# Performance work log

Measured on AMD Instinct MI355X. Metric: run time of the kernel, lower is better.

## Reference

```python
import jax, jax.numpy as jnp
import numpy as np

N_NODES = 50000
N_EDGES = 1_600_000
IN_C, HID_C, OUT_C = 512, 256, 50
ALPHA = 0.1
NUM_LAYERS = 10


def setup_inputs() -> dict:
    key = jax.random.key(0)
    ks = jax.random.split(key, 8)
    x = jax.random.normal(ks[0], (N_NODES, IN_C), dtype=jnp.float32)
    edge_row = jax.random.randint(ks[1], (N_EDGES,), 0, N_NODES, dtype=jnp.int32)
    edge_col = jax.random.randint(ks[2], (N_EDGES,), 0, N_NODES, dtype=jnp.int32)
    edge_weight = jax.random.uniform(ks[3], (N_EDGES,), dtype=jnp.float32)
    s1 = 1.0 / np.sqrt(IN_C)
    s2 = 1.0 / np.sqrt(HID_C)
    W1 = jax.random.uniform(ks[4], (IN_C, HID_C), minval=-s1, maxval=s1, dtype=jnp.float32)
    b1 = jax.random.uniform(ks[5], (HID_C,), minval=-s1, maxval=s1, dtype=jnp.float32)
    W2 = jax.random.uniform(ks[6], (HID_C, OUT_C), minval=-s2, maxval=s2, dtype=jnp.float32)
    b2 = jax.random.uniform(ks[7], (OUT_C,), minval=-s2, maxval=s2, dtype=jnp.float32)
    return {"x": x, "edge_row": edge_row, "edge_col": edge_col,
            "edge_weight": edge_weight, "W1": W1, "b1": b1, "W2": W2, "b2": b2}


def reference(x, edge_row, edge_col, edge_weight, W1, b1, W2, b2):
    # MLP: Linear -> ReLU -> Linear (dropout inactive in eval, no batch norm)
    h = jax.nn.relu(x @ W1 + b1)          # [N, HID_C]
    h = h @ W2 + b2                        # [N, OUT_C]
    x0 = h

    def spmm(v):
        # out[i] = sum_{e: row[e]==i} w[e] * v[col[e]]
        msgs = v[edge_col] * edge_weight[:, None]   # [E, OUT_C]
        return jax.ops.segment_sum(msgs, edge_row, num_segments=N_NODES)

    def step(h, _):
        h = spmm(h) * (1.0 - ALPHA) + ALPHA * x0
        return h, None

    h, _ = jax.lax.scan(step, h, None, length=NUM_LAYERS)
    return jax.nn.log_softmax(h, axis=1)
```

## Files before the change

### kernel.cpp

```cpp
#include <hip/hip_runtime.h>
#include <cstddef>
#include <cstdint>
#include <math.h>

#define N_NODES 50000
#define N_EDGES 1600000
#define IN_C 512
#define HID_C 256
#define OUT_C 50
#define PAD_C 64
#define NUM_LAYERS 10
#define NBUCK 98
#define BSHIFT 9
#define BCAP 20480
#define PHB_CHUNK 8192
#define PHB_BLOCKS 196
#define TW_BLOCKS 128
#define PW_BLOCKS 64
#define GEMM_BLOCKS 782

typedef __attribute__((ext_vector_type(8))) short short8;
typedef __attribute__((ext_vector_type(4))) float floatx4;

__device__ inline unsigned short f2bf(float f) {
    unsigned int u = __float_as_uint(f);
    u += 0x7fffu + ((u >> 16) & 1u);
    return (unsigned short)(u >> 16);
}

__device__ inline unsigned cvtpk(float lo, float hi) {
    unsigned r;
    asm("v_cvt_pk_bf16_f32 %0, %1, %2" : "=v"(r) : "v"(lo), "v"(hi));
    return r;
}

__device__ inline short8 pack_bf16x8(float4 lo, float4 hi) {
    union { unsigned u[4]; short8 s; } r;
    r.u[0] = cvtpk(lo.x, lo.y);
    r.u[1] = cvtpk(lo.z, lo.w);
    r.u[2] = cvtpk(hi.x, hi.y);
    r.u[3] = cvtpk(hi.z, hi.w);
    return r.s;
}

#define ASYNC16(g, l)                                                     \
    __builtin_amdgcn_global_load_lds(                                     \
        (const __attribute__((address_space(1))) void*)(g),               \
        (__attribute__((address_space(3))) void*)(l), 16, 0, 0)

#define WAITCNT6() asm volatile("s_waitcnt vmcnt(6)" ::: "memory")
#define WAITCNT0() asm volatile("s_waitcnt vmcnt(0)" ::: "memory")
#define SBAR()     __builtin_amdgcn_s_barrier()

__global__ __launch_bounds__(256) void prep_fused(const int* __restrict__ erow,
                                                  const int* __restrict__ ecol,
                                                  const float* __restrict__ ew,
                                                  int* __restrict__ bfill,
                                                  uint2* __restrict__ buckets,
                                                  const float* __restrict__ W1,
                                                  unsigned short* __restrict__ Wt,
                                                  const float* __restrict__ W2,
                                                  const float* __restrict__ b2,
                                                  unsigned short* __restrict__ Wpt,
                                                  float* __restrict__ bp) {
    __shared__ int  lcnt[NBUCK];
    __shared__ int  lbase[NBUCK];
    __shared__ float tile[32][33];
    const int bid = blockIdx.x;
    const int t = threadIdx.x;

    if (bid < PHB_BLOCKS) {
        for (int b = t; b < NBUCK; b += 256) lcnt[b] = 0;
        __syncthreads();
        const int e0 = bid * PHB_CHUNK;
        const int e1 = min(e0 + PHB_CHUNK, N_EDGES);
        for (int e = e0 + t; e < e1; e += 256)
            atomicAdd(&lcnt[erow[e] >> BSHIFT], 1);
        __syncthreads();
        for (int b = t; b < NBUCK; b += 256) {
            lbase[b] = atomicAdd(&bfill[b], lcnt[b]);
            lcnt[b] = 0;
        }
        __syncthreads();
        for (int e = e0 + t; e < e1; e += 256) {
            int r = erow[e];
            int b = r >> BSHIFT;
            int o = atomicAdd(&lcnt[b], 1);
            int idx = lbase[b] + o;
            if (idx < BCAP) {
                unsigned packed = ((unsigned)(r - (b << BSHIFT)) << 17) | (unsigned)ecol[e];
                buckets[(size_t)b * BCAP + idx] = make_uint2(packed, __float_as_uint(ew[e]));
            }
        }
    } else if (bid < PHB_BLOCKS + TW_BLOCKS) {
        int tb = bid - PHB_BLOCKS;
        int bx = tb & 15;
        int by = tb >> 4;
        int tx = t & 31, ty = t >> 5;
#pragma unroll
        for (int i = 0; i < 32; i += 8)
            tile[ty + i][tx] = W1[(bx * 32 + ty + i) * HID_C + by * 32 + tx];
        __syncthreads();
#pragma unroll
        for (int i = 0; i < 32; i += 8)
            Wt[(size_t)(by * 32 + ty + i) * IN_C + bx * 32 + tx] = f2bf(tile[tx][ty + i]);
    } else {
        int idx = (bid - PHB_BLOCKS - TW_BLOCKS) * 256 + t;
        if (idx < PAD_C * HID_C) {
            int n = idx >> 8, k = idx & 255;
            float v = (n < OUT_C) ? W2[k * OUT_C + n] : 0.f;
            Wpt[idx] = f2bf(v);
        }
        if (idx < PAD_C) bp[idx] = (idx < OUT_C) ? b2[idx] : 0.f;
    }
}

__global__ __launch_bounds__(128) void bucket_scan(const int* __restrict__ bfill,
                                                   int* __restrict__ bbase,
                                                   int* __restrict__ rowptr) {
    __shared__ int sd[128];
    int t = threadIdx.x;
    int v = (t < NBUCK) ? min(bfill[t], BCAP) : 0;
    sd[t] = v;
    __syncthreads();
    for (int off = 1; off < 128; off <<= 1) {
        int x = (t >= off) ? sd[t - off] : 0;
        __syncthreads();
        sd[t] += x;
        __syncthreads();
    }
    if (t < NBUCK) bbase[t] = sd[t] - v;
    if (t == NBUCK - 1) {
        bbase[NBUCK] = sd[t];
        rowptr[N_NODES] = sd[t];
    }
}

__global__ __launch_bounds__(256) void csr_gemm_fused(
        const uint2* __restrict__ buckets, const int* __restrict__ bfill,
        const int* __restrict__ bbase, int* __restrict__ rowptr,
        uint2* __restrict__ edges,
        const float* __restrict__ A, const unsigned short* __restrict__ Wt,
        const float* __restrict__ b1, const unsigned short* __restrict__ Wpt,
        const float* __restrict__ bp, unsigned short* __restrict__ h0b) {
    __shared__ __align__(16) char smem[73728];
    const int bid = blockIdx.x;
    const int tid = threadIdx.x;

    if (bid < NBUCK) {
        int* hist = (int*)smem;
        int* excl = (int*)(smem + 2048);
        int* psum = (int*)(smem + 4096);
        const int b = bid;
        const int t = tid;
        const int n = min(bfill[b], BCAP);
        const uint2* bk = buckets + (size_t)b * BCAP;

        hist[t] = 0; hist[t + 256] = 0;
        __syncthreads();
        for (int i = t; i < n; i += 256)
            atomicAdd(&hist[bk[i].x >> 17], 1);
        __syncthreads();
        int a0 = hist[2 * t], a1 = hist[2 * t + 1];
        psum[t] = a0 + a1;
        __syncthreads();
        for (int off = 1; off < 256; off <<= 1) {
            int x = (t >= off) ? psum[t - off] : 0;
            __syncthreads();
            psum[t] += x;
            __syncthreads();
        }
        int pe = psum[t] - (a0 + a1);
        excl[2 * t] = pe;
        excl[2 * t + 1] = pe + a0;
        __syncthreads();
        const int base = bbase[b];
#pragma unroll
        for (int k = 0; k < 2; ++k) {
            int lr = t + k * 256;
            int r = (b << BSHIFT) + lr;
            if (r < N_NODES) rowptr[r] = base + excl[lr];
        }
        hist[t] = 0; hist[t + 256] = 0;
        __syncthreads();
        for (int i = t; i < n; i += 256) {
            uint2 ed = bk[i];
            int lr = ed.x >> 17;
            int pos = base + excl[lr] + atomicAdd(&hist[lr], 1);
            edges[pos] = make_uint2(ed.x & 0x1FFFFu, ed.y);
        }
        return;
    }

    float*          Ab[3] = {(float*)smem,
                             (float*)(smem + 24576),
                             (float*)(smem + 49152)};
    unsigned short* Bb[3] = {(unsigned short*)(smem + 8192),
                             (unsigned short*)(smem + 32768),
                             (unsigned short*)(smem + 57344)};
    unsigned short* Hs = (unsigned short*)smem;
    const int HS_LD = 264;

    const int wave = tid >> 6, lane = tid & 63;
    const int quad = lane >> 4, l16 = lane & 15;
    const int m0 = (bid - NBUCK) * 64;
    const int wm = (wave >> 1) * 32;
    const int wn = (wave & 1) * 128;

    floatx4 acc[2][8];
#pragma unroll
    for (int i = 0; i < 2; ++i)
#pragma unroll
        for (int j = 0; j < 8; ++j) acc[i][j] = (floatx4){0.f, 0.f, 0.f, 0.f};

    auto stage = [&](int bi, int ks) {
        const int k0 = ks << 5;
#pragma unroll
        for (int j = 0; j < 2; ++j) {
            int slot = tid + j * 256;
            int r = slot >> 3, c = slot & 7;
            int gr = m0 + r;
            if (gr >= N_NODES) gr = N_NODES - 1;
            const float* src = A + (size_t)gr * IN_C + k0 + ((c ^ (r & 7)) << 2);
            ASYNC16(src, Ab[bi] + (slot << 2));
        }
#pragma unroll
        for (int j = 0; j < 4; ++j) {
            int slot = tid + j * 256;
            int n = slot >> 2, c = slot & 3;
            int cs = c ^ ((n >> 1) & 3);
            const unsigned short* src = Wt + (size_t)n * IN_C + k0 + (cs << 3);
            ASYNC16(src, Bb[bi] + (slot << 3));
        }
    };

    auto compute = [&](int bi) {
        const float* As_ = Ab[bi];
        const unsigned short* Bs_ = Bb[bi];
        short8 bfr[8], afr[2];
#pragma unroll
        for (int nt = 0; nt < 8; ++nt) {
            int n  = wn + nt * 16 + l16;
            int cq = quad ^ ((n >> 1) & 3);
            bfr[nt] = *(const short8*)&Bs_[(n << 5) + (cq << 3)];
        }
#pragma unroll
        for (int mt = 0; mt < 2; ++mt) {
            int r  = wm + mt * 16 + l16;
            int rx = r & 7;
            float4 lo = *(const float4*)&As_[(r << 5) + (((2 * quad)     ^ rx) << 2)];
            float4 hi = *(const float4*)&As_[(r << 5) + (((2 * quad + 1) ^ rx) << 2)];
            afr[mt] = pack_bf16x8(lo, hi);
        }
#pragma unroll
        for (int mt = 0; mt < 2; ++mt)
#pragma unroll
            for (int nt = 0; nt < 8; ++nt)
                acc[mt][nt] = __builtin_amdgcn_mfma_f32_16x16x32_bf16(afr[mt], bfr[nt],
                                                                      acc[mt][nt], 0, 0, 0);
    };

    stage(0, 0);
    stage(1, 1);
#pragma unroll
    for (int ks = 0; ks < 14; ++ks) {
        WAITCNT6();
        SBAR();
        stage((ks + 2) % 3, ks + 2);
        compute(ks % 3);
    }
    WAITCNT6(); SBAR(); compute(2);
    WAITCNT0(); SBAR(); compute(0);
    __syncthreads();

#pragma unroll
    for (int nt = 0; nt < 8; ++nt) {
        int n = wn + nt * 16 + l16;
        float bn = b1[n];
#pragma unroll
        for (int mt = 0; mt < 2; ++mt)
#pragma unroll
            for (int r = 0; r < 4; ++r) {
                float v = acc[mt][nt][r] + bn;
                v = v > 0.f ? v : 0.f;
                Hs[(wm + mt * 16 + quad * 4 + r) * HS_LD + n] = f2bf(v);
            }
    }
    __syncthreads();

    floatx4 acc2[4];
#pragma unroll
    for (int nt = 0; nt < 4; ++nt) acc2[nt] = (floatx4){0.f, 0.f, 0.f, 0.f};
    const int hrow = (wave << 4) + l16;
#pragma unroll
    for (int k2 = 0; k2 < 8; ++k2) {
        short8 haf = *(const short8*)&Hs[hrow * HS_LD + (k2 << 5) + (quad << 3)];
#pragma unroll
        for (int nt = 0; nt < 4; ++nt) {
            short8 bf = *(const short8*)&Wpt[(size_t)((nt << 4) + l16) * HID_C + (k2 << 5) + (quad << 3)];
            acc2[nt] = __builtin_amdgcn_mfma_f32_16x16x32_bf16(haf, bf, acc2[nt], 0, 0, 0);
        }
    }
#pragma unroll
    for (int nt = 0; nt < 4; ++nt) {
        int c = (nt << 4) + l16;
        float bn = bp[c];
#pragma unroll
        for (int r = 0; r < 4; ++r) {
            int row = m0 + (wave << 4) + (quad << 2) + r;
            if (row < N_NODES)
                h0b[(size_t)row * PAD_C + c] = f2bf(acc2[nt][r] + bn);
        }
    }
}

__device__ inline void edge_fma(float* acc, float wgt, uint4 hv) {
    acc[0] = fmaf(wgt, __uint_as_float(hv.x << 16),         acc[0]);
    acc[1] = fmaf(wgt, __uint_as_float(hv.x & 0xffff0000u), acc[1]);
    acc[2] = fmaf(wgt, __uint_as_float(hv.y << 16),         acc[2]);
    acc[3] = fmaf(wgt, __uint_as_float(hv.y & 0xffff0000u), acc[3]);
    acc[4] = fmaf(wgt, __uint_as_float(hv.z << 16),         acc[4]);
    acc[5] = fmaf(wgt, __uint_as_float(hv.z & 0xffff0000u), acc[5]);
    acc[6] = fmaf(wgt, __uint_as_float(hv.w << 16),         acc[6]);
    acc[7] = fmaf(wgt, __uint_as_float(hv.w & 0xffff0000u), acc[7]);
}

template <bool LAST>
__global__ __launch_bounds__(256, 8) void prop8(const int* __restrict__ rowptr,
                                                const uint2* __restrict__ edges,
                                                const unsigned short* __restrict__ hin,
                                                const unsigned short* __restrict__ h0b,
                                                unsigned short* __restrict__ hout_b,
                                                float* __restrict__ out_f) {
    int wid = (blockIdx.x * blockDim.x + threadIdx.x) >> 6;
    if (wid >= N_NODES) return;
    int lane = threadIdx.x & 63;
    int slot = lane >> 3;
    int lc   = lane & 7;
    int s = rowptr[wid], e = rowptr[wid + 1];

    float acc0[8], acc1[8];
#pragma unroll
    for (int k = 0; k < 8; ++k) { acc0[k] = 0.f; acc1[k] = 0.f; }

    int i = s;
    for (; i + 32 <= e; i += 32) {
        uint2 cw0 = edges[i + slot];
        uint2 cw1 = edges[i + 8 + slot];
        uint2 cw2 = edges[i + 16 + slot];
        uint2 cw3 = edges[i + 24 + slot];
        uint4 hv0 = *(const uint4*)((const char*)hin + ((size_t)cw0.x << 7) + lc * 16);
        uint4 hv1 = *(const uint4*)((const char*)hin + ((size_t)cw1.x << 7) + lc * 16);
        uint4 hv2 = *(const uint4*)((const char*)hin + ((size_t)cw2.x << 7) + lc * 16);
        uint4 hv3 = *(const uint4*)((const char*)hin + ((size_t)cw3.x << 7) + lc * 16);
        edge_fma(acc0, __uint_as_float(cw0.y), hv0);
        edge_fma(acc1, __uint_as_float(cw1.y), hv1);
        edge_fma(acc0, __uint_as_float(cw2.y), hv2);
        edge_fma(acc1, __uint_as_float(cw3.y), hv3);
    }
    for (; i + 16 <= e; i += 16) {
        uint2 cw0 = edges[i + slot];
        uint2 cw1 = edges[i + 8 + slot];
        uint4 hv0 = *(const uint4*)((const char*)hin + ((size_t)cw0.x << 7) + lc * 16);
        uint4 hv1 = *(const uint4*)((const char*)hin + ((size_t)cw1.x << 7) + lc * 16);
        edge_fma(acc0, __uint_as_float(cw0.y), hv0);
        edge_fma(acc1, __uint_as_float(cw1.y), hv1);
    }
    for (; i < e; i += 8) {
        int idx = i + slot;
        uint2 cw = (idx < e) ? edges[idx] : make_uint2(0u, 0u);
        float wgt = (idx < e) ? __uint_as_float(cw.y) : 0.f;
        uint4 hv = *(const uint4*)((const char*)hin + ((size_t)cw.x << 7) + lc * 16);
        edge_fma(acc0, wgt, hv);
    }

    float r[8];
#pragma unroll
    for (int k = 0; k < 8; ++k) {
        float v = acc0[k] + acc1[k];
        v += __shfl_xor(v, 8, 64);
        v += __shfl_xor(v, 16, 64);
        v += __shfl_xor(v, 32, 64);
        r[k] = v;
    }

    uint4 h0v = *(const uint4*)((const char*)h0b + ((size_t)wid << 7) + lc * 16);
    float h0e[8];
    h0e[0] = __uint_as_float(h0v.x << 16);
    h0e[1] = __uint_as_float(h0v.x & 0xffff0000u);
    h0e[2] = __uint_as_float(h0v.y << 16);
    h0e[3] = __uint_as_float(h0v.y & 0xffff0000u);
    h0e[4] = __uint_as_float(h0v.z << 16);
    h0e[5] = __uint_as_float(h0v.z & 0xffff0000u);
    h0e[6] = __uint_as_float(h0v.w << 16);
    h0e[7] = __uint_as_float(h0v.w & 0xffff0000u);
#pragma unroll
    for (int k = 0; k < 8; ++k) r[k] = 0.9f * r[k] + 0.1f * h0e[k];

    if (!LAST) {
        if (slot == 0) {
            uint4 u;
            u.x = ((unsigned)f2bf(r[1]) << 16) | f2bf(r[0]);
            u.y = ((unsigned)f2bf(r[3]) << 16) | f2bf(r[2]);
            u.z = ((unsigned)f2bf(r[5]) << 16) | f2bf(r[4]);
            u.w = ((unsigned)f2bf(r[7]) << 16) | f2bf(r[6]);
            *(uint4*)((char*)hout_b + ((size_t)wid << 7) + lc * 16) = u;
        }
    } else {
        int ch0 = lc * 8;
        float m = -INFINITY;
#pragma unroll
        for (int k = 0; k < 8; ++k) if (ch0 + k < OUT_C) m = fmaxf(m, r[k]);
        m = fmaxf(m, __shfl_xor(m, 1, 64));
        m = fmaxf(m, __shfl_xor(m, 2, 64));
        m = fmaxf(m, __shfl_xor(m, 4, 64));
        float ss = 0.f;
#pragma unroll
        for (int k = 0; k < 8; ++k) if (ch0 + k < OUT_C) ss += __expf(r[k] - m);
        ss += __shfl_xor(ss, 1, 64);
        ss += __shfl_xor(ss, 2, 64);
        ss += __shfl_xor(ss, 4, 64);
        float lse = __logf(ss);
        if (slot == 0) {
#pragma unroll
            for (int k = 0; k < 8; ++k)
                if (ch0 + k < OUT_C)
                    out_f[(size_t)wid * OUT_C + ch0 + k] = (r[k] - m) - lse;
        }
    }
}

extern "C" void kernel_launch(void* const* d_in, const int* in_sizes, int n_in,
                              void* d_out, int out_size, void* d_ws, size_t ws_size,
                              hipStream_t stream) {
    const float* x    = (const float*)d_in[0];
    const int*   erow = (const int*)d_in[1];
    const int*   ecol = (const int*)d_in[2];
    const float* ew   = (const float*)d_in[3];
    const float* W1   = (const float*)d_in[4];
    const float* b1   = (const float*)d_in[5];
    const float* W2   = (const float*)d_in[6];
    const float* b2   = (const float*)d_in[7];
    float* out = (float*)d_out;

    char* p = (char*)d_ws;
    auto alloc = [&](size_t bytes) {
        char* r = p;
        p += (bytes + 255) & ~(size_t)255;
        return r;
    };
    char*  scratch = alloc((size_t)NBUCK * BCAP * 8);
    unsigned short* h0b = (unsigned short*)alloc((size_t)N_NODES * PAD_C * 2);
    uint2* edges  = (uint2*)alloc((size_t)N_EDGES * 8);
    int*   rowptr = (int*)alloc((size_t)(N_NODES + 1) * 4);
    int*   bfill  = (int*)alloc((size_t)NBUCK * 4);
    int*   bbase  = (int*)alloc((size_t)(NBUCK + 1) * 4);
    float* bp     = (float*)alloc((size_t)PAD_C * 4);
    unsigned short* Wt  = (unsigned short*)alloc((size_t)HID_C * IN_C * 2);
    unsigned short* Wpt = (unsigned short*)alloc((size_t)PAD_C * HID_C * 2);
    uint2* buckets = (uint2*)scratch;
    unsigned short* ha = (unsigned short*)scratch;
    unsigned short* hb = (unsigned short*)(scratch + (size_t)N_NODES * PAD_C * 2);

    hipMemsetAsync(bfill, 0, (size_t)NBUCK * 4, stream);

    prep_fused<<<PHB_BLOCKS + TW_BLOCKS + PW_BLOCKS, 256, 0, stream>>>(
        erow, ecol, ew, bfill, buckets, W1, Wt, W2, b2, Wpt, bp);

    bucket_scan<<<1, 128, 0, stream>>>(bfill, bbase, rowptr);

    csr_gemm_fused<<<NBUCK + GEMM_BLOCKS, 256, 0, stream>>>(
        buckets, bfill, bbase, rowptr, edges,
        x, Wt, b1, Wpt, bp, h0b);

    const int prop_blocks = (N_NODES * 64 + 255) / 256;
    const unsigned short* cur = h0b;
    unsigned short* nxt = ha;
    for (int l = 0; l < NUM_LAYERS - 1; ++l) {
        prop8<false><<<prop_blocks, 256, 0, stream>>>(rowptr, edges, cur, h0b,
                                                      nxt, nullptr);
        const unsigned short* t = nxt;
        nxt = (nxt == ha) ? hb : ha;
        cur = t;
    }
    prop8<true><<<prop_blocks, 256, 0, stream>>>(rowptr, edges, cur, h0b,
                                                 nullptr, out);
}
```

Baseline: 560.8 us.

## Store propagation features as scaled FP8 with per-layer amax tracking

Intermediate propagation features move from bf16 (128 B per node) to FP8 E4M3 (64 B per node). Each layer's values are scaled by a running absolute maximum recorded through atomics in the GEMM epilogue and in each propagation layer. The gather kernel is remapped to 16 edges per wave with 16 channels per lane, dequantising with packed FP8-to-F32 conversions. This targets the memory-bound random gathers in the SpMM loop. It adds quantisation error that can compound over ten layers, and relies on a scale taken from the previous layer's maximum staying within FP8 range.

```diff
diff --git a/kernel.cpp b/kernel.cpp
--- a/kernel.cpp
+++ b/kernel.cpp
@@ -21,6 +21,7 @@
 
 typedef __attribute__((ext_vector_type(8))) short short8;
 typedef __attribute__((ext_vector_type(4))) float floatx4;
+typedef __attribute__((ext_vector_type(2))) float floatx2;
 
 __device__ inline unsigned short f2bf(float f) {
     unsigned int u = __float_as_uint(f);
@@ -41,6 +42,27 @@
     r.u[2] = cvtpk(hi.x, hi.y);
     r.u[3] = cvtpk(hi.z, hi.w);
     return r.s;
+}
+
+__device__ inline void fp8x4_fma(float wgt, unsigned w, float* acc) {
+    floatx2 lo = __builtin_amdgcn_cvt_pk_f32_fp8(w, false);
+    floatx2 hi = __builtin_amdgcn_cvt_pk_f32_fp8(w, true);
+    acc[0] = fmaf(wgt, lo[0], acc[0]);
+    acc[1] = fmaf(wgt, lo[1], acc[1]);
+    acc[2] = fmaf(wgt, hi[0], acc[2]);
+    acc[3] = fmaf(wgt, hi[1], acc[3]);
+}
+__device__ inline void fp8_fma16(float* acc, float wgt, uint4 hv) {
+    fp8x4_fma(wgt, hv.x, acc + 0);
+    fp8x4_fma(wgt, hv.y, acc + 4);
+    fp8x4_fma(wgt, hv.z, acc + 8);
+    fp8x4_fma(wgt, hv.w, acc + 12);
+}
+__device__ inline unsigned pack_fp8x4(float a, float b, float c, float d) {
+    int r = 0;
+    r = __builtin_amdgcn_cvt_pk_fp8_f32(a, b, r, false);
+    r = __builtin_amdgcn_cvt_pk_fp8_f32(c, d, r, true);
+    return (unsigned)r;
 }
 
 #define ASYNC16(g, l)                                                     \
@@ -142,7 +164,8 @@
         uint2* __restrict__ edges,
         const float* __restrict__ A, const unsigned short* __restrict__ Wt,
         const float* __restrict__ b1, const unsigned short* __restrict__ Wpt,
-        const float* __restrict__ bp, unsigned short* __restrict__ h0b) {
+        const float* __restrict__ bp, unsigned short* __restrict__ h0b,
+        unsigned* __restrict__ amax) {
     __shared__ __align__(16) char smem[73728];
     const int bid = blockIdx.x;
     const int tid = threadIdx.x;
@@ -301,6 +324,7 @@
             acc2[nt] = __builtin_amdgcn_mfma_f32_16x16x32_bf16(haf, bf, acc2[nt], 0, 0, 0);
         }
     }
+    float vmax = 0.f;
 #pragma unroll
     for (int nt = 0; nt < 4; ++nt) {
         int c = (nt << 4) + l16;
@@ -308,11 +332,17 @@
 #pragma unroll
         for (int r = 0; r < 4; ++r) {
             int row = m0 + (wave << 4) + (quad << 2) + r;
+            float v = acc2[nt][r] + bn;
+            vmax = fmaxf(vmax, fabsf(v));
             if (row < N_NODES)
-                h0b[(size_t)row * PAD_C + c] = f2bf(acc2[nt][r] + bn);
-        }
-    }
-}
+                h0b[(size_t)row * PAD_C + c] = f2bf(v);
+        }
+    }
+#pragma unroll
+    for (int s = 1; s < 64; s <<= 1) vmax = fmaxf(vmax, __shfl_xor(vmax, s, 64));
+    if (lane == 0) atomicMax(&amax[0], __float_as_uint(vmax));
+}
+
 
 __device__ inline void edge_fma(float* acc, float wgt, uint4 hv) {
     acc[0] = fmaf(wgt, __uint_as_float(hv.x << 16),         acc[0]);
@@ -325,13 +355,11 @@
     acc[7] = fmaf(wgt, __uint_as_float(hv.w & 0xffff0000u), acc[7]);
 }
 
-template <bool LAST>
-__global__ __launch_bounds__(256, 8) void prop8(const int* __restrict__ rowptr,
+__global__ __launch_bounds__(256, 8) void prop0(const int* __restrict__ rowptr,
                                                 const uint2* __restrict__ edges,
-                                                const unsigned short* __restrict__ hin,
                                                 const unsigned short* __restrict__ h0b,
-                                                unsigned short* __restrict__ hout_b,
-                                                float* __restrict__ out_f) {
+                                                unsigned* __restrict__ amax,
+                                                unsigned char* __restrict__ tout) {
     int wid = (blockIdx.x * blockDim.x + threadIdx.x) >> 6;
     if (wid >= N_NODES) return;
     int lane = threadIdx.x & 63;
@@ -349,10 +377,10 @@
         uint2 cw1 = edges[i + 8 + slot];
         uint2 cw2 = edges[i + 16 + slot];
         uint2 cw3 = edges[i + 24 + slot];
-        uint4 hv0 = *(const uint4*)((const char*)hin + ((size_t)cw0.x << 7) + lc * 16);
-        uint4 hv1 = *(const uint4*)((const char*)hin + ((size_t)cw1.x << 7) + lc * 16);
-        uint4 hv2 = *(const uint4*)((const char*)hin + ((size_t)cw2.x << 7) + lc * 16);
-        uint4 hv3 = *(const uint4*)((const char*)hin + ((size_t)cw3.x << 7) + lc * 16);
+        uint4 hv0 = *(const uint4*)((const char*)h0b + ((size_t)cw0.x << 7) + lc * 16);
+        uint4 hv1 = *(const uint4*)((const char*)h0b + ((size_t)cw1.x << 7) + lc * 16);
+        uint4 hv2 = *(const uint4*)((const char*)h0b + ((size_t)cw2.x << 7) + lc * 16);
+        uint4 hv3 = *(const uint4*)((const char*)h0b + ((size_t)cw3.x << 7) + lc * 16);
         edge_fma(acc0, __uint_as_float(cw0.y), hv0);
         edge_fma(acc1, __uint_as_float(cw1.y), hv1);
         edge_fma(acc0, __uint_as_float(cw2.y), hv2);
@@ -361,8 +389,8 @@
     for (; i + 16 <= e; i += 16) {
         uint2 cw0 = edges[i + slot];
         uint2 cw1 = edges[i + 8 + slot];
-        uint4 hv0 = *(const uint4*)((const char*)hin + ((size_t)cw0.x << 7) + lc * 16);
-        uint4 hv1 = *(const uint4*)((const char*)hin + ((size_t)cw1.x << 7) + lc * 16);
+        uint4 hv0 = *(const uint4*)((const char*)h0b + ((size_t)cw0.x << 7) + lc * 16);
+        uint4 hv1 = *(const uint4*)((const char*)h0b + ((size_t)cw1.x << 7) + lc * 16);
         edge_fma(acc0, __uint_as_float(cw0.y), hv0);
         edge_fma(acc1, __uint_as_float(cw1.y), hv1);
     }
@@ -370,7 +398,7 @@
         int idx = i + slot;
         uint2 cw = (idx < e) ? edges[idx] : make_uint2(0u, 0u);
         float wgt = (idx < e) ? __uint_as_float(cw.y) : 0.f;
-        uint4 hv = *(const uint4*)((const char*)hin + ((size_t)cw.x << 7) + lc * 16);
+        uint4 hv = *(const uint4*)((const char*)h0b + ((size_t)cw.x << 7) + lc * 16);
         edge_fma(acc0, wgt, hv);
     }
 
@@ -397,35 +425,127 @@
 #pragma unroll
     for (int k = 0; k < 8; ++k) r[k] = 0.9f * r[k] + 0.1f * h0e[k];
 
+    float s_out = 4.0f / __uint_as_float(amax[0]);
+    if (slot == 0) {
+        uint2 u;
+        u.x = pack_fp8x4(r[0] * s_out, r[1] * s_out, r[2] * s_out, r[3] * s_out);
+        u.y = pack_fp8x4(r[4] * s_out, r[5] * s_out, r[6] * s_out, r[7] * s_out);
+        *(uint2*)(tout + (size_t)wid * 64 + lc * 8) = u;
+    }
+    float vmax = 0.f;
+#pragma unroll
+    for (int k = 0; k < 8; ++k) vmax = fmaxf(vmax, fabsf(r[k]));
+    vmax = fmaxf(vmax, __shfl_xor(vmax, 1, 64));
+    vmax = fmaxf(vmax, __shfl_xor(vmax, 2, 64));
+    vmax = fmaxf(vmax, __shfl_xor(vmax, 4, 64));
+    if (lane == 0) {
+        unsigned cur = __hip_atomic_load(&amax[1], __ATOMIC_RELAXED, __HIP_MEMORY_SCOPE_AGENT);
+        if (vmax > __uint_as_float(cur)) atomicMax(&amax[1], __float_as_uint(vmax));
+    }
+}
+
+template <bool LAST>
+__global__ __launch_bounds__(256, 8) void prop_fp8(const int* __restrict__ rowptr,
+                                                   const uint2* __restrict__ edges,
+                                                   const unsigned char* __restrict__ tin,
+                                                   const unsigned short* __restrict__ h0b,
+                                                   unsigned* __restrict__ amax,
+                                                   const int l,
+                                                   unsigned char* __restrict__ tout,
+                                                   float* __restrict__ out_f) {
+    int wid = (blockIdx.x * blockDim.x + threadIdx.x) >> 6;
+    if (wid >= N_NODES) return;
+    int lane = threadIdx.x & 63;
+    int slot = lane >> 2;
+    int lc2  = lane & 3;
+    int s = rowptr[wid], e = rowptr[wid + 1];
+
+    float acc[16];
+#pragma unroll
+    for (int k = 0; k < 16; ++k) acc[k] = 0.f;
+
+    int i = s;
+    for (; i + 32 <= e; i += 32) {
+        uint2 cw0 = edges[i + slot];
+        uint2 cw1 = edges[i + 16 + slot];
+        uint4 hv0 = *(const uint4*)(tin + ((size_t)cw0.x << 6) + lc2 * 16);
+        uint4 hv1 = *(const uint4*)(tin + ((size_t)cw1.x << 6) + lc2 * 16);
+        fp8_fma16(acc, __uint_as_float(cw0.y), hv0);
+        fp8_fma16(acc, __uint_as_float(cw1.y), hv1);
+    }
+    for (; i < e; i += 16) {
+        int idx = i + slot;
+        uint2 cw = (idx < e) ? edges[idx] : make_uint2(0u, 0u);
+        float wgt = (idx < e) ? __uint_as_float(cw.y) : 0.f;
+        uint4 hv = *(const uint4*)(tin + ((size_t)cw.x << 6) + lc2 * 16);
+        fp8_fma16(acc, wgt, hv);
+    }
+
+    const float inv_sin = __uint_as_float(amax[l - 1]) * 0.25f;
+
+    float r[16];
+#pragma unroll
+    for (int k = 0; k < 16; ++k) {
+        float v = acc[k];
+        v += __shfl_xor(v, 4, 64);
+        v += __shfl_xor(v, 8, 64);
+        v += __shfl_xor(v, 16, 64);
+        v += __shfl_xor(v, 32, 64);
+        r[k] = v;
+    }
+
+    uint4 ha = *(const uint4*)((const char*)h0b + ((size_t)wid << 7) + lc2 * 32);
+    uint4 hb = *(const uint4*)((const char*)h0b + ((size_t)wid << 7) + lc2 * 32 + 16);
+    float h0e[16];
+    h0e[0]  = __uint_as_float(ha.x << 16); h0e[1]  = __uint_as_float(ha.x & 0xffff0000u);
+    h0e[2]  = __uint_as_float(ha.y << 16); h0e[3]  = __uint_as_float(ha.y & 0xffff0000u);
+    h0e[4]  = __uint_as_float(ha.z << 16); h0e[5]  = __uint_as_float(ha.z & 0xffff0000u);
+    h0e[6]  = __uint_as_float(ha.w << 16); h0e[7]  = __uint_as_float(ha.w & 0xffff0000u);
+    h0e[8]  = __uint_as_float(hb.x << 16); h0e[9]  = __uint_as_float(hb.x & 0xffff0000u);
+    h0e[10] = __uint_as_float(hb.y << 16); h0e[11] = __uint_as_float(hb.y & 0xffff0000u);
+    h0e[12] = __uint_as_float(hb.z << 16); h0e[13] = __uint_as_float(hb.z & 0xffff0000u);
+    h0e[14] = __uint_as_float(hb.w << 16); h0e[15] = __uint_as_float(hb.w & 0xffff0000u);
+#pragma unroll
+    for (int k = 0; k < 16; ++k) r[k] = 0.9f * inv_sin * r[k] + 0.1f * h0e[k];
+
     if (!LAST) {
+        float s_out = 4.0f / __uint_as_float(amax[l]);
         if (slot == 0) {
             uint4 u;
-            u.x = ((unsigned)f2bf(r[1]) << 16) | f2bf(r[0]);
-            u.y = ((unsigned)f2bf(r[3]) << 16) | f2bf(r[2]);
-            u.z = ((unsigned)f2bf(r[5]) << 16) | f2bf(r[4]);
-            u.w = ((unsigned)f2bf(r[7]) << 16) | f2bf(r[6]);
-            *(uint4*)((char*)hout_b + ((size_t)wid << 7) + lc * 16) = u;
+            u.x = pack_fp8x4(r[0]*s_out,  r[1]*s_out,  r[2]*s_out,  r[3]*s_out);
+            u.y = pack_fp8x4(r[4]*s_out,  r[5]*s_out,  r[6]*s_out,  r[7]*s_out);
+            u.z = pack_fp8x4(r[8]*s_out,  r[9]*s_out,  r[10]*s_out, r[11]*s_out);
+            u.w = pack_fp8x4(r[12]*s_out, r[13]*s_out, r[14]*s_out, r[15]*s_out);
+            *(uint4*)(tout + (size_t)wid * 64 + lc2 * 16) = u;
+        }
+        float vmax = 0.f;
+#pragma unroll
+        for (int k = 0; k < 16; ++k) vmax = fmaxf(vmax, fabsf(r[k]));
+        vmax = fmaxf(vmax, __shfl_xor(vmax, 1, 64));
+        vmax = fmaxf(vmax, __shfl_xor(vmax, 2, 64));
+        if (lane == 0) {
+            unsigned cur = __hip_atomic_load(&amax[l + 1], __ATOMIC_RELAXED,
+                                             __HIP_MEMORY_SCOPE_AGENT);
+            if (vmax > __uint_as_float(cur)) atomicMax(&amax[l + 1], __float_as_uint(vmax));
         }
     } else {
-        int ch0 = lc * 8;
+        const int nval = (lc2 == 3) ? 2 : 16;
         float m = -INFINITY;
 #pragma unroll
-        for (int k = 0; k < 8; ++k) if (ch0 + k < OUT_C) m = fmaxf(m, r[k]);
+        for (int k = 0; k < 16; ++k) if (k < nval) m = fmaxf(m, r[k]);
         m = fmaxf(m, __shfl_xor(m, 1, 64));
         m = fmaxf(m, __shfl_xor(m, 2, 64));
-        m = fmaxf(m, __shfl_xor(m, 4, 64));
         float ss = 0.f;
 #pragma unroll
-        for (int k = 0; k < 8; ++k) if (ch0 + k < OUT_C) ss += __expf(r[k] - m);
+        for (int k = 0; k < 16; ++k) if (k < nval) ss += __expf(r[k] - m);
         ss += __shfl_xor(ss, 1, 64);
         ss += __shfl_xor(ss, 2, 64);
-        ss += __shfl_xor(ss, 4, 64);
         float lse = __logf(ss);
         if (slot == 0) {
 #pragma unroll
-            for (int k = 0; k < 8; ++k)
-                if (ch0 + k < OUT_C)
-                    out_f[(size_t)wid * OUT_C + ch0 + k] = (r[k] - m) - lse;
+            for (int k = 0; k < 16; ++k)
+                if (k < nval)
+                    out_f[(size_t)wid * OUT_C + lc2 * 16 + k] = (r[k] - m) - lse;
         }
     }
 }
@@ -455,14 +575,16 @@
     int*   rowptr = (int*)alloc((size_t)(N_NODES + 1) * 4);
     int*   bfill  = (int*)alloc((size_t)NBUCK * 4);
     int*   bbase  = (int*)alloc((size_t)(NBUCK + 1) * 4);
+    unsigned* amax = (unsigned*)alloc(64);
     float* bp     = (float*)alloc((size_t)PAD_C * 4);
     unsigned short* Wt  = (unsigned short*)alloc((size_t)HID_C * IN_C * 2);
     unsigned short* Wpt = (unsigned short*)alloc((size_t)PAD_C * HID_C * 2);
     uint2* buckets = (uint2*)scratch;
-    unsigned short* ha = (unsigned short*)scratch;
-    unsigned short* hb = (unsigned short*)(scratch + (size_t)N_NODES * PAD_C * 2);
+    unsigned char* ta = (unsigned char*)scratch;
+    unsigned char* tb = (unsigned char*)(scratch + (size_t)N_NODES * 64);
 
     hipMemsetAsync(bfill, 0, (size_t)NBUCK * 4, stream);
+    hipMemsetAsync(amax, 0, 64, stream);
 
     prep_fused<<<PHB_BLOCKS + TW_BLOCKS + PW_BLOCKS, 256, 0, stream>>>(
         erow, ecol, ew, bfill, buckets, W1, Wt, W2, b2, Wpt, bp);
@@ -471,18 +593,17 @@
 
     csr_gemm_fused<<<NBUCK + GEMM_BLOCKS, 256, 0, stream>>>(
         buckets, bfill, bbase, rowptr, edges,
-        x, Wt, b1, Wpt, bp, h0b);
+        x, Wt, b1, Wpt, bp, h0b, amax);
 
     const int prop_blocks = (N_NODES * 64 + 255) / 256;
-    const unsigned short* cur = h0b;
-    unsigned short* nxt = ha;
-    for (int l = 0; l < NUM_LAYERS - 1; ++l) {
-        prop8<false><<<prop_blocks, 256, 0, stream>>>(rowptr, edges, cur, h0b,
-                                                      nxt, nullptr);
-        const unsigned short* t = nxt;
-        nxt = (nxt == ha) ? hb : ha;
-        cur = t;
-    }
-    prop8<true><<<prop_blocks, 256, 0, stream>>>(rowptr, edges, cur, h0b,
-                                                 nullptr, out);
-}
+    prop0<<<prop_blocks, 256, 0, stream>>>(rowptr, edges, h0b, amax, ta);
+    unsigned char* cur = ta;
+    unsigned char* nxt = tb;
+    for (int l = 1; l <= 8; ++l) {
+        prop_fp8<false><<<prop_blocks, 256, 0, stream>>>(rowptr, edges, cur, h0b,
+                                                         amax, l, nxt, nullptr);
+        unsigned char* t = cur; cur = nxt; nxt = t;
+    }
+    prop_fp8<true><<<prop_blocks, 256, 0, stream>>>(rowptr, edges, cur, h0b,
+                                                    amax, 9, nullptr, out);
+}
```

After: 784.4 us. 1.4x slower.
